# Performance work log

Hardware: AMD Instinct MI355X
Metric: run time of the kernel (lower is better)

The kernel has to match this reference:

```python
import jax, jax.numpy as jnp
import numpy as np
from jax import lax

HIDDEN = 256
WIDTH = 1024
DEPTH = 4
T = 64
SUBSTEPS = 8  # fixed RK4 substeps per save interval (replaces diffrax adaptive Tsit5)

Y0 = np.array([0.0008417, 0.01495894, 0.00082556, 0.00068982, 0.00063456,
               0.00832867, 0.00190631, 0.00155624, 0.00142264, 0.01858621,
               0.02000239, 0.01796071, 0.01670121, 0.22218046, 0.02531468,
               0.03337227, 0.6147068], dtype=np.float32)


def setup_inputs() -> dict:
    key = jax.random.key(0)
    ks = jax.random.split(key, 8)

    def lin(k, out, inp):
        kw, kb = jax.random.split(k)
        lim = 1.0 / np.sqrt(inp)
        W = jax.random.uniform(kw, (out, inp), jnp.float32, -lim, lim)
        b = jax.random.uniform(kb, (out,), jnp.float32, -lim, lim)
        return W, b

    W0, b0 = lin(ks[0], WIDTH, HIDDEN + 17)
    Whs, bhs = [], []
    for i in range(DEPTH - 1):
        w, b = lin(ks[1 + i], WIDTH, WIDTH)
        Whs.append(w)
        bhs.append(b)
    Wh = jnp.stack(Whs)   # [DEPTH-1, WIDTH, WIDTH]
    bh = jnp.stack(bhs)   # [DEPTH-1, WIDTH]
    Wl, bl = lin(ks[4], HIDDEN, WIDTH)
    beta_W, beta_b = lin(ks[5], 1, HIDDEN)
    hvec = 0.01 * jax.random.normal(ks[6], (HIDDEN,), jnp.float32)
    scale = jnp.array([0.1], jnp.float32)
    y0_log = jnp.log(jnp.asarray(Y0))
    ts = jnp.arange(T, dtype=jnp.float32) * 0.25  # save points (months)
    return dict(ts=ts, W0=W0, b0=b0, Wh=Wh, bh=bh, Wl=Wl, bl=bl,
                beta_W=beta_W, beta_b=beta_b, hvec=hvec, scale=scale,
                y0_log=y0_log)


def _forward(ts, W0, b0, Wh, bh, Wl, bl, beta_W, beta_b, hvec, scale, y0_log):
    xi, mu, sigma, nu, gamma = 13/12, 0.041/12, 91/12, 36/12, 1.8/12

    def mlp(x):  # softplus hidden activations, final tanh(0.01*x)
        z = jax.nn.softplus(W0 @ x + b0)
        def body(z, wb):
            w, b = wb
            return jax.nn.softplus(w @ z + b), None
        z, _ = lax.scan(body, z, (Wh, bh))
        return jnp.tanh(0.01 * (Wl @ z + bl))

    def rhs(y):  # y = concat(state[17], h[HIDDEN])
        state, h = y[:17], y[17:]
        bb1 = 8.0 * jax.nn.sigmoid(beta_W @ h + beta_b)[0] + 25.0
        bb2, bb3, bb4 = 0.5 * bb1, 0.35 * bb1, 0.25 * bb1
        M, S1, E1, E2, E3, E4, I1, I2, I3, I4, R1, R2, R3, R4, S2, S3, S4 = state
        I = I1 + I2 + I3 + I4
        R = R1 + R2 + R3 + R4
        dstate = jnp.stack([
            R * mu - (xi + mu) * M,
            mu * (1 - R) + xi * M - mu * S1 - bb1 * I * S1,
            bb1 * I * S1 - (mu + sigma) * E1,
            bb2 * I * S2 - (mu + sigma) * E2,
            bb3 * I * S3 - (mu + sigma) * E3,
            bb4 * I * S4 - (mu + sigma) * E4,
            sigma * E1 - (nu + mu) * I1,
            sigma * E2 - (nu + mu) * I2,
            sigma * E3 - (nu + mu) * I3,
            sigma * E4 - (nu + mu) * I4,
            nu * I1 - (mu + gamma) * R1,
            nu * I2 - (mu + gamma) * R2,
            nu * I3 - (mu + gamma) * R3,
            nu * I4 - (mu + gamma) * R4,
            gamma * R1 - mu * S2 - bb2 * I * S2,
            gamma * R2 - mu * S3 - bb3 * I * S3,
            gamma * (R3 + R4) - mu * S4 - bb4 * I * S4,
        ])
        dh = scale[0] * mlp(jnp.concatenate([h, state]))
        return jnp.concatenate([dstate, dh])

    def rk4(y, dt):
        k1 = rhs(y)
        k2 = rhs(y + 0.5 * dt * k1)
        k3 = rhs(y + 0.5 * dt * k2)
        k4 = rhs(y + dt * k3)
        return y + (dt / 6.0) * (k1 + 2 * k2 + 2 * k3 + k4)

    y0 = jnp.concatenate([jax.nn.softmax(y0_log), hvec])

    def interval(y, dt_i):
        dt = dt_i / SUBSTEPS
        def step(y, _):
            return rk4(y, dt), None
        y, _ = lax.scan(step, y, None, length=SUBSTEPS)
        return y, y

    dts = ts[1:] - ts[:-1]
    _, ys = lax.scan(interval, y0, dts)
    ys = jnp.concatenate([y0[None], ys], axis=0)  # [T, 17+HIDDEN]
    return ys[:, :17], ys[:, 17:]


def reference(ts, W0, b0, Wh, bh, Wl, bl, beta_W, beta_b, hvec, scale, y0_log):
    return _forward(ts, W0, b0, Wh, bh, Wl, bl, beta_W, beta_b, hvec, scale, y0_log)
```

## Files before the change

### kernel.cpp

```cpp
#include <hip/hip_runtime.h>
#include <math.h>

#define NBLK    32
#define NLAUNCH 256
#define BS      512
#define NSTATE  17
#define NH      256
#define NX      273
#define WID     1024
#define NT      64
#define NSUB    8
#define SLC     32
#define POLL_CAP 2000000

#define SCALE_H 16777216.0f
#define INV_H   5.9604644775390625e-8f
#define SCALE_D 1048576.0f
#define INV_D   9.5367431640625e-7f

typedef unsigned long long u64;
typedef unsigned int u32;

__device__ __forceinline__ float softplus_f(float v) {
    return fmaxf(v, 0.f) + log1pf(expf(-fabsf(v)));
}

__device__ __forceinline__ void acc_add(u64* p, float v, float scale) {
    long long q = llrintf(v * scale);
    u64 w = ((u64)q << 16) + 1ULL;
    asm volatile("global_atomic_add_x2 %0, %1, off" :: "v"(p), "v"(w) : "memory");
}
__device__ __forceinline__ u64 rmw_read(const u64* p) {
    u64 w;
    asm volatile("global_atomic_add_x2 %0, %1, %2, off sc0\n\t"
                 "s_waitcnt vmcnt(0)"
                 : "=&v"(w) : "v"(p), "v"(0ULL) : "memory");
    return w;
}
__device__ __forceinline__ void reset_word(u64* p) {
    asm volatile("global_atomic_swap_x2 %0, %1, off" :: "v"(p), "v"(0ULL) : "memory");
}

extern "C" __global__ __launch_bounds__(BS, 1) void ode_kernel(
    const float* __restrict__ ts,   const float* __restrict__ W0,
    const float* __restrict__ b0,   const float* __restrict__ Wh,
    const float* __restrict__ bh,   const float* __restrict__ Wl,
    const float* __restrict__ bl,   const float* __restrict__ betaW,
    const float* __restrict__ betab,const float* __restrict__ hvec,
    const float* __restrict__ scale,const float* __restrict__ y0log,
    float* __restrict__ out, u64* hacc1, u64* hacc2, u64* hacc3,
    u64* dhacc, unsigned* ctrl)
{
    const int t = threadIdx.x;

    __shared__ int role_sh;
    __shared__ __align__(16) float y_s[NX];
    __shared__ __align__(16) float yn_s[NX];
    __shared__ __align__(16) float xm[NX];
    __shared__ __align__(16) float k_s[NX];
    __shared__ __align__(16) float z1_s[SLC];
    __shared__ __align__(16) float h1_s[SLC];
    __shared__ __align__(16) float h2_s[SLC];
    __shared__ __align__(16) float h3_s[SLC];
    __shared__ float red[8];
    __shared__ float dt_sh;
    extern __shared__ float wh3c[];

    if (t == 0) {
        int xcd;
        asm volatile("s_getreg_b32 %0, hwreg(HW_REG_XCC_ID)" : "=s"(xcd));
        xcd &= 7;
        unsigned rk = atomicAdd(&ctrl[xcd], 1u);
        if (rk == NBLK - 1) atomicCAS(&ctrl[8], 0u, (unsigned)(xcd + 1));
        unsigned w; int it = 0;
        do {
            w = __hip_atomic_load(&ctrl[8], __ATOMIC_RELAXED, __HIP_MEMORY_SCOPE_AGENT);
        } while (w == 0u && ++it < POLL_CAP);
        role_sh = (w != 0u && xcd == (int)w - 1 && rk < NBLK) ? (int)rk : -1;
    }
    __syncthreads();
    const int blk = role_sh;
    if (blk < 0) return;

    const float scale0 = scale[0];
    const float betab0 = betab[0];

    const int rowH = t >> 4, laneH = t & 15;
    const int growH = blk * SLC + rowH;

    const float b0r    = b0[growH];
    const float betaWr = (t < NH) ? betaW[t] : 0.f;
    const float blr    = (t < NH) ? bl[t] : 0.f;
    float bhc[3];
    if (t < SLC) {
        bhc[0] = bh[blk * SLC + t];
        bhc[1] = bh[WID + blk * SLC + t];
        bhc[2] = bh[2 * WID + blk * SLC + t];
    }

    float w0r[18];
    {
        const float* w0p = W0 + (size_t)growH * NX;
        #pragma unroll
        for (int i = 0; i < 18; i++) {
            int c = laneH + i * 16;
            w0r[i] = (c < NX) ? w0p[c] : 0.f;
        }
    }
    float4 wc1a[8], wc1b[8], wc2a[8], wc2b[8];
    {
        const float* base0 = Wh + (size_t)t * WID + blk * SLC;
        const float* base1 = Wh + (size_t)(t + 512) * WID + blk * SLC;
        #pragma unroll
        for (int q = 0; q < 8; q++) {
            wc1a[q] = *(const float4*)(base0 + q * 4);
            wc1b[q] = *(const float4*)(base1 + q * 4);
            wc2a[q] = *(const float4*)(base0 + (size_t)WID * WID + q * 4);
            wc2b[q] = *(const float4*)(base1 + (size_t)WID * WID + q * 4);
        }
    }
    {
        const float* src = Wh + 2 * (size_t)WID * WID;
        for (int i = t; i < WID * 8; i += BS) {
            int r = i >> 3, q = i & 7;
            float4 v = *(const float4*)(src + (size_t)r * WID + blk * SLC + q * 4);
            wh3c[(q * 4 + 0) * WID + r] = v.x;
            wh3c[(q * 4 + 1) * WID + r] = v.y;
            wh3c[(q * 4 + 2) * WID + r] = v.z;
            wh3c[(q * 4 + 3) * WID + r] = v.w;
        }
    }

    if (t < NSTATE) {
        float m = -1e30f;
        for (int j = 0; j < NSTATE; j++) m = fmaxf(m, y0log[j]);
        float ssum = 0.f;
        for (int j = 0; j < NSTATE; j++) ssum += expf(y0log[j] - m);
        y_s[t] = expf(y0log[t] - m) / ssum;
    }
    if (t < NH) y_s[NSTATE + t] = hvec[t];
    __syncthreads();

    if (blk == 0) {
        if (t < NSTATE) out[t] = y_s[t];
        if (t < NH)     out[NT * NSTATE + t] = y_s[NSTATE + t];
    }

    const float c_xi = 13.f / 12.f, c_mu = 0.041f / 12.f, c_sig = 91.f / 12.f,
                c_nu = 36.f / 12.f, c_gam = 1.8f / 12.f;

    long long prev_dh = 0;
    unsigned sidx = 0;

    for (int iv = 0; iv < NT - 1; iv++) {
        if (t == 0) dt_sh = (ts[iv + 1] - ts[iv]) * (1.f / NSUB);
        __syncthreads();
        const float dt = dt_sh;

        for (int sub = 0; sub < NSUB; sub++) {
            if (t < NX) yn_s[t] = y_s[t];

            for (int s = 0; s < 4; s++) {
                const float a   = (s == 0) ? 0.f : ((s == 3) ? 1.f : 0.5f);
                const float wgt = ((s == 0) || (s == 3)) ? dt * (1.f / 6.f) : dt * (1.f / 3.f);
                const float adt = a * dt;
                ++sidx;

                if (t < NX) {
                    const int src = (t < NH) ? (NSTATE + t) : (t - NH);
                    float v = y_s[src];
                    if (s != 0) v = fmaf(adt, k_s[src], v);
                    xm[t] = v;
                }
                __syncthreads();

                {
                    float acc = 0.f;
                    #pragma unroll
                    for (int i = 0; i < 18; i++) {
                        int c = laneH + i * 16;
                        if (c < NX) acc = fmaf(w0r[i], xm[c], acc);
                    }
                    #pragma unroll
                    for (int m = 1; m < 16; m <<= 1) acc += __shfl_xor(acc, m, 16);
                    if (laneH == 0) z1_s[rowH] = softplus_f(acc + b0r);
                }
                if (t < NH) {
                    float p = betaWr * xm[t];
                    #pragma unroll
                    for (int m = 1; m < 64; m <<= 1) p += __shfl_xor(p, m, 64);
                    if ((t & 63) == 0) red[t >> 6] = p;
                }
                __syncthreads();

                {
                    float p0 = 0.f, p1 = 0.f;
                    #pragma unroll
                    for (int q = 0; q < 8; q++) {
                        float4 z = *(const float4*)(z1_s + q * 4);
                        p0 = fmaf(wc1a[q].x, z.x, p0); p0 = fmaf(wc1a[q].y, z.y, p0);
                        p0 = fmaf(wc1a[q].z, z.z, p0); p0 = fmaf(wc1a[q].w, z.w, p0);
                        p1 = fmaf(wc1b[q].x, z.x, p1); p1 = fmaf(wc1b[q].y, z.y, p1);
                        p1 = fmaf(wc1b[q].z, z.z, p1); p1 = fmaf(wc1b[q].w, z.w, p1);
                    }
                    acc_add(hacc1 + t, p0, SCALE_H);
                    acc_add(hacc1 + t + 512, p1, SCALE_H);
                }

                if (t == 256) {
                    const float* xs = xm + NH;
                    float sd  = red[0] + red[1] + red[2] + red[3] + betab0;
                    float bb1 = 8.f / (1.f + expf(-sd)) + 25.f;
                    float bb2 = 0.5f * bb1, bb3 = 0.35f * bb1, bb4 = 0.25f * bb1;
                    float M  = xs[0],  S1 = xs[1],  E1 = xs[2],  E2 = xs[3];
                    float E3 = xs[4],  E4 = xs[5],  I1 = xs[6],  I2 = xs[7];
                    float I3 = xs[8],  I4 = xs[9],  R1 = xs[10], R2 = xs[11];
                    float R3 = xs[12], R4 = xs[13], S2 = xs[14], S3 = xs[15];
                    float S4 = xs[16];
                    float I = I1 + I2 + I3 + I4, Rs = R1 + R2 + R3 + R4;
                    k_s[0]  = Rs * c_mu - (c_xi + c_mu) * M;
                    k_s[1]  = c_mu * (1.f - Rs) + c_xi * M - c_mu * S1 - bb1 * I * S1;
                    k_s[2]  = bb1 * I * S1 - (c_mu + c_sig) * E1;
                    k_s[3]  = bb2 * I * S2 - (c_mu + c_sig) * E2;
                    k_s[4]  = bb3 * I * S3 - (c_mu + c_sig) * E3;
                    k_s[5]  = bb4 * I * S4 - (c_mu + c_sig) * E4;
                    k_s[6]  = c_sig * E1 - (c_nu + c_mu) * I1;
                    k_s[7]  = c_sig * E2 - (c_nu + c_mu) * I2;
                    k_s[8]  = c_sig * E3 - (c_nu + c_mu) * I3;
                    k_s[9]  = c_sig * E4 - (c_nu + c_mu) * I4;
                    k_s[10] = c_nu * I1 - (c_mu + c_gam) * R1;
                    k_s[11] = c_nu * I2 - (c_mu + c_gam) * R2;
                    k_s[12] = c_nu * I3 - (c_mu + c_gam) * R3;
                    k_s[13] = c_nu * I4 - (c_mu + c_gam) * R4;
                    k_s[14] = c_gam * R1 - c_mu * S2 - bb2 * I * S2;
                    k_s[15] = c_gam * R2 - c_mu * S3 - bb3 * I * S3;
                    k_s[16] = c_gam * (R3 + R4) - c_mu * S4 - bb4 * I * S4;
                }

                if (t < SLC) {
                    u64* p = hacc1 + blk * SLC + t;
                    u64 w; int it = 0;
                    do { w = rmw_read(p); } while ((w & 0xFFFFu) != 32u && ++it < POLL_CAP);
                    reset_word(p);
                    asm volatile("s_waitcnt vmcnt(0)" ::: "memory");
                    long long val = ((long long)w) >> 16;
                    h1_s[t] = softplus_f((float)val * INV_H + bhc[0]);
                }
                __syncthreads();

                {
                    float p0 = 0.f, p1 = 0.f;
                    #pragma unroll
                    for (int q = 0; q < 8; q++) {
                        float4 z = *(const float4*)(h1_s + q * 4);
                        p0 = fmaf(wc2a[q].x, z.x, p0); p0 = fmaf(wc2a[q].y, z.y, p0);
                        p0 = fmaf(wc2a[q].z, z.z, p0); p0 = fmaf(wc2a[q].w, z.w, p0);
                        p1 = fmaf(wc2b[q].x, z.x, p1); p1 = fmaf(wc2b[q].y, z.y, p1);
                        p1 = fmaf(wc2b[q].z, z.z, p1); p1 = fmaf(wc2b[q].w, z.w, p1);
                    }
                    acc_add(hacc2 + t, p0, SCALE_H);
                    acc_add(hacc2 + t + 512, p1, SCALE_H);
                }
                if (t < SLC) {
                    u64* p = hacc2 + blk * SLC + t;
                    u64 w; int it = 0;
                    do { w = rmw_read(p); } while ((w & 0xFFFFu) != 32u && ++it < POLL_CAP);
                    reset_word(p);
                    asm volatile("s_waitcnt vmcnt(0)" ::: "memory");
                    long long val = ((long long)w) >> 16;
                    h2_s[t] = softplus_f((float)val * INV_H + bhc[1]);
                }
                __syncthreads();

                {
                    float p0 = 0.f, p1 = 0.f;
                    #pragma unroll
                    for (int j = 0; j < SLC; j++) {
                        float hv = h2_s[j];
                        p0 = fmaf(wh3c[j * WID + t],       hv, p0);
                        p1 = fmaf(wh3c[j * WID + t + 512], hv, p1);
                    }
                    acc_add(hacc3 + t, p0, SCALE_H);
                    acc_add(hacc3 + t + 512, p1, SCALE_H);
                }
                float4 wvL[8];
                if (t < NH) {
                    const float* wp = Wl + (size_t)t * WID + blk * SLC;
                    #pragma unroll
                    for (int q = 0; q < 8; q++) wvL[q] = *(const float4*)(wp + q * 4);
                }
                if (t < SLC) {
                    u64* p = hacc3 + blk * SLC + t;
                    u64 w; int it = 0;
                    do { w = rmw_read(p); } while ((w & 0xFFFFu) != 32u && ++it < POLL_CAP);
                    reset_word(p);
                    asm volatile("s_waitcnt vmcnt(0)" ::: "memory");
                    long long val = ((long long)w) >> 16;
                    h3_s[t] = softplus_f((float)val * INV_H + bhc[2]);
                }
                __syncthreads();

                if (t < NH) {
                    float p = 0.f;
                    #pragma unroll
                    for (int q = 0; q < 8; q++) {
                        float4 z = *(const float4*)(h3_s + q * 4);
                        p = fmaf(wvL[q].x, z.x, p); p = fmaf(wvL[q].y, z.y, p);
                        p = fmaf(wvL[q].z, z.z, p); p = fmaf(wvL[q].w, z.w, p);
                    }
                    acc_add(dhacc + t, p, SCALE_D);

                    u64* dp = dhacc + t;
                    const u32 tgt = (32u * sidx) & 0xFFFFu;
                    u64 w; int it = 0;
                    do { w = rmw_read(dp); } while ((u32)(w & 0xFFFFu) != tgt && ++it < POLL_CAP);
                    long long val = ((long long)w) >> 16;
                    long long diff = val - prev_dh;
                    prev_dh = val;
                    float accv = (float)diff * INV_D;
                    k_s[NSTATE + t] = scale0 * tanhf(0.01f * (accv + blr));
                }
                __syncthreads();
                if (t < NX) yn_s[t] = fmaf(wgt, k_s[t], yn_s[t]);
            }

            __syncthreads();
            if (t < NX) y_s[t] = yn_s[t];
            __syncthreads();
        }

        if (blk == 0) {
            if (t < NSTATE) out[(iv + 1) * NSTATE + t] = y_s[t];
            if (t < NH)     out[NT * NSTATE + (iv + 1) * NH + t] = y_s[NSTATE + t];
        }
    }
}

extern "C" void kernel_launch(void* const* d_in, const int* in_sizes, int n_in,
                              void* d_out, int out_size, void* d_ws, size_t ws_size,
                              hipStream_t stream) {
    const float* ts    = (const float*)d_in[0];
    const float* W0    = (const float*)d_in[1];
    const float* b0    = (const float*)d_in[2];
    const float* Wh    = (const float*)d_in[3];
    const float* bh    = (const float*)d_in[4];
    const float* Wl    = (const float*)d_in[5];
    const float* bl    = (const float*)d_in[6];
    const float* betaW = (const float*)d_in[7];
    const float* betab = (const float*)d_in[8];
    const float* hvec  = (const float*)d_in[9];
    const float* scale = (const float*)d_in[10];
    const float* y0log = (const float*)d_in[11];
    float* out = (float*)d_out;

    u64*      hacc1 = (u64*)d_ws;
    u64*      hacc2 = (u64*)((char*)d_ws + 8192);
    u64*      hacc3 = (u64*)((char*)d_ws + 16384);
    u64*      dhacc = (u64*)((char*)d_ws + 24576);
    unsigned* ctrl  = (unsigned*)((char*)d_ws + 26624);

    static int lds_set = 0;
    if (!lds_set) {
        hipFuncSetAttribute((const void*)ode_kernel,
                            hipFuncAttributeMaxDynamicSharedMemorySize, 131072);
        lds_set = 1;
    }

    hipMemsetAsync(d_ws, 0, 26624 + 64, stream);
    hipLaunchKernelGGL(ode_kernel, dim3(NLAUNCH), dim3(BS), 131072, stream,
                       ts, W0, b0, Wh, bh, Wl, bl, betaW, betab, hvec, scale,
                       y0log, out, hacc1, hacc2, hacc3, dhacc, ctrl);
}
```

Measured before the change: 23.76 ms.

## Pack two fixed-point partial sums per atomic and double-buffer accumulators

Hidden-layer partial sums for two adjacent rows are now packed into one 64-bit atomic word: an 8-bit arrival counter plus two biased 28-bit fixed-point values at a coarser scale. This halves the atomic traffic and the number of polled words per block. Accumulator buffers alternate by stage parity, so the reset swap no longer has to be waited on before continuing. Row mapping changes to adjacent row pairs, and the Wh3 read becomes a float2 load. The trade is reduced precision (scale 2^15, 28-bit range), a risk of overflow or accuracy loss, and a need for double-sized accumulator buffers.

```diff
diff --git a/kernel.cpp b/kernel.cpp
--- a/kernel.cpp
+++ b/kernel.cpp
@@ -13,8 +13,10 @@
 #define SLC     32
 #define POLL_CAP 2000000
 
-#define SCALE_H 16777216.0f
-#define INV_H   5.9604644775390625e-8f
+#define SCALE_P 32768.0f
+#define INV_P   3.0517578125e-5f
+#define BIAS_P  (1LL << 22)
+#define BIAS32  (32LL << 22)
 #define SCALE_D 1048576.0f
 #define INV_D   9.5367431640625e-7f
 
@@ -25,8 +27,14 @@
     return fmaxf(v, 0.f) + log1pf(expf(-fabsf(v)));
 }
 
-__device__ __forceinline__ void acc_add(u64* p, float v, float scale) {
-    long long q = llrintf(v * scale);
+__device__ __forceinline__ void acc_pack(u64* p, float p0, float p1) {
+    long long q0 = llrintf(p0 * SCALE_P) + BIAS_P;
+    long long q1 = llrintf(p1 * SCALE_P) + BIAS_P;
+    u64 w = 1ULL + ((u64)q0 << 8) + ((u64)q1 << 36);
+    asm volatile("global_atomic_add_x2 %0, %1, off" :: "v"(p), "v"(w) : "memory");
+}
+__device__ __forceinline__ void acc_dh(u64* p, float v) {
+    long long q = llrintf(v * SCALE_D);
     u64 w = ((u64)q << 16) + 1ULL;
     asm volatile("global_atomic_add_x2 %0, %1, off" :: "v"(p), "v"(w) : "memory");
 }
@@ -37,7 +45,7 @@
                  : "=&v"(w) : "v"(p), "v"(0ULL) : "memory");
     return w;
 }
-__device__ __forceinline__ void reset_word(u64* p) {
+__device__ __forceinline__ void reset_async(u64* p) {
     asm volatile("global_atomic_swap_x2 %0, %1, off" :: "v"(p), "v"(0ULL) : "memory");
 }
 
@@ -87,15 +95,20 @@
 
     const int rowH = t >> 4, laneH = t & 15;
     const int growH = blk * SLC + rowH;
+    const int r0 = 2 * t, r1 = 2 * t + 1;
 
     const float b0r    = b0[growH];
     const float betaWr = (t < NH) ? betaW[t] : 0.f;
     const float blr    = (t < NH) ? bl[t] : 0.f;
     float bhc[3];
-    if (t < SLC) {
-        bhc[0] = bh[blk * SLC + t];
-        bhc[1] = bh[WID + blk * SLC + t];
-        bhc[2] = bh[2 * WID + blk * SLC + t];
+    float bhc_o[3];
+    if (t < 16) {
+        bhc[0]   = bh[blk * SLC + 2 * t];
+        bhc_o[0] = bh[blk * SLC + 2 * t + 1];
+        bhc[1]   = bh[WID + blk * SLC + 2 * t];
+        bhc_o[1] = bh[WID + blk * SLC + 2 * t + 1];
+        bhc[2]   = bh[2 * WID + blk * SLC + 2 * t];
+        bhc_o[2] = bh[2 * WID + blk * SLC + 2 * t + 1];
     }
 
     float w0r[18];
@@ -109,8 +122,8 @@
     }
     float4 wc1a[8], wc1b[8], wc2a[8], wc2b[8];
     {
-        const float* base0 = Wh + (size_t)t * WID + blk * SLC;
-        const float* base1 = Wh + (size_t)(t + 512) * WID + blk * SLC;
+        const float* base0 = Wh + (size_t)r0 * WID + blk * SLC;
+        const float* base1 = Wh + (size_t)r1 * WID + blk * SLC;
         #pragma unroll
         for (int q = 0; q < 8; q++) {
             wc1a[q] = *(const float4*)(base0 + q * 4);
@@ -165,6 +178,10 @@
                 const float wgt = ((s == 0) || (s == 3)) ? dt * (1.f / 6.f) : dt * (1.f / 3.f);
                 const float adt = a * dt;
                 ++sidx;
+                const int par = (int)(sidx & 1u);
+                u64* h1p = hacc1 + par * 512;
+                u64* h2p = hacc2 + par * 512;
+                u64* h3p = hacc3 + par * 512;
 
                 if (t < NX) {
                     const int src = (t < NH) ? (NSTATE + t) : (t - NH);
@@ -203,8 +220,7 @@
                         p1 = fmaf(wc1b[q].x, z.x, p1); p1 = fmaf(wc1b[q].y, z.y, p1);
                         p1 = fmaf(wc1b[q].z, z.z, p1); p1 = fmaf(wc1b[q].w, z.w, p1);
                     }
-                    acc_add(hacc1 + t, p0, SCALE_H);
-                    acc_add(hacc1 + t + 512, p1, SCALE_H);
+                    acc_pack(h1p + t, p0, p1);
                 }
 
                 if (t == 256) {
@@ -237,14 +253,15 @@
                     k_s[16] = c_gam * (R3 + R4) - c_mu * S4 - bb4 * I * S4;
                 }
 
-                if (t < SLC) {
-                    u64* p = hacc1 + blk * SLC + t;
+                if (t < 16) {
+                    u64* p = h1p + blk * 16 + t;
                     u64 w; int it = 0;
-                    do { w = rmw_read(p); } while ((w & 0xFFFFu) != 32u && ++it < POLL_CAP);
-                    reset_word(p);
-                    asm volatile("s_waitcnt vmcnt(0)" ::: "memory");
-                    long long val = ((long long)w) >> 16;
-                    h1_s[t] = softplus_f((float)val * INV_H + bhc[0]);
+                    do { w = rmw_read(p); } while ((w & 0xFFu) != 32u && ++it < POLL_CAP);
+                    reset_async(p);
+                    long long v0 = (long long)((w >> 8) & 0xFFFFFFFULL) - BIAS32;
+                    long long v1 = (long long)(w >> 36) - BIAS32;
+                    h1_s[2 * t]     = softplus_f((float)v0 * INV_P + bhc[0]);
+                    h1_s[2 * t + 1] = softplus_f((float)v1 * INV_P + bhc_o[0]);
                 }
                 __syncthreads();
 
@@ -258,17 +275,17 @@
                         p1 = fmaf(wc2b[q].x, z.x, p1); p1 = fmaf(wc2b[q].y, z.y, p1);
                         p1 = fmaf(wc2b[q].z, z.z, p1); p1 = fmaf(wc2b[q].w, z.w, p1);
                     }
-                    acc_add(hacc2 + t, p0, SCALE_H);
-                    acc_add(hacc2 + t + 512, p1, SCALE_H);
-                }
-                if (t < SLC) {
-                    u64* p = hacc2 + blk * SLC + t;
+                    acc_pack(h2p + t, p0, p1);
+                }
+                if (t < 16) {
+                    u64* p = h2p + blk * 16 + t;
                     u64 w; int it = 0;
-                    do { w = rmw_read(p); } while ((w & 0xFFFFu) != 32u && ++it < POLL_CAP);
-                    reset_word(p);
-                    asm volatile("s_waitcnt vmcnt(0)" ::: "memory");
-                    long long val = ((long long)w) >> 16;
-                    h2_s[t] = softplus_f((float)val * INV_H + bhc[1]);
+                    do { w = rmw_read(p); } while ((w & 0xFFu) != 32u && ++it < POLL_CAP);
+                    reset_async(p);
+                    long long v0 = (long long)((w >> 8) & 0xFFFFFFFULL) - BIAS32;
+                    long long v1 = (long long)(w >> 36) - BIAS32;
+                    h2_s[2 * t]     = softplus_f((float)v0 * INV_P + bhc[1]);
+                    h2_s[2 * t + 1] = softplus_f((float)v1 * INV_P + bhc_o[1]);
                 }
                 __syncthreads();
 
@@ -277,11 +294,11 @@
                     #pragma unroll
                     for (int j = 0; j < SLC; j++) {
                         float hv = h2_s[j];
-                        p0 = fmaf(wh3c[j * WID + t],       hv, p0);
-                        p1 = fmaf(wh3c[j * WID + t + 512], hv, p1);
-                    }
-                    acc_add(hacc3 + t, p0, SCALE_H);
-                    acc_add(hacc3 + t + 512, p1, SCALE_H);
+                        float2 wv = *(const float2*)(wh3c + j * WID + r0);
+                        p0 = fmaf(wv.x, hv, p0);
+                        p1 = fmaf(wv.y, hv, p1);
+                    }
+                    acc_pack(h3p + t, p0, p1);
                 }
                 float4 wvL[8];
                 if (t < NH) {
@@ -289,14 +306,15 @@
                     #pragma unroll
                     for (int q = 0; q < 8; q++) wvL[q] = *(const float4*)(wp + q * 4);
                 }
-                if (t < SLC) {
-                    u64* p = hacc3 + blk * SLC + t;
+                if (t < 16) {
+                    u64* p = h3p + blk * 16 + t;
                     u64 w; int it = 0;
-                    do { w = rmw_read(p); } while ((w & 0xFFFFu) != 32u && ++it < POLL_CAP);
-                    reset_word(p);
-                    asm volatile("s_waitcnt vmcnt(0)" ::: "memory");
-                    long long val = ((long long)w) >> 16;
-                    h3_s[t] = softplus_f((float)val * INV_H + bhc[2]);
+                    do { w = rmw_read(p); } while ((w & 0xFFu) != 32u && ++it < POLL_CAP);
+                    reset_async(p);
+                    long long v0 = (long long)((w >> 8) & 0xFFFFFFFULL) - BIAS32;
+                    long long v1 = (long long)(w >> 36) - BIAS32;
+                    h3_s[2 * t]     = softplus_f((float)v0 * INV_P + bhc[2]);
+                    h3_s[2 * t + 1] = softplus_f((float)v1 * INV_P + bhc_o[2]);
                 }
                 __syncthreads();
 
@@ -308,7 +326,7 @@
                         p = fmaf(wvL[q].x, z.x, p); p = fmaf(wvL[q].y, z.y, p);
                         p = fmaf(wvL[q].z, z.z, p); p = fmaf(wvL[q].w, z.w, p);
                     }
-                    acc_add(dhacc + t, p, SCALE_D);
+                    acc_dh(dhacc + t, p);
 
                     u64* dp = dhacc + t;
                     const u32 tgt = (32u * sidx) & 0xFFFFu;
```

New measurement: 21.15 ms. 1.12x faster.
